# Kernel tuning notes

Measured on AMD Instinct MI355X. Metric: run time of the kernel, lower is better.

Reference implementation:

```python
import jax, jax.numpy as jnp
import numpy as np

NOISE_EPS = 0.01
TOP_K = 2


def setup_inputs() -> dict:
    key = jax.random.key(0)
    k1, k2, k3, k4 = jax.random.split(key, 4)
    B, S, D, E = 4, 4096, 2048, 64
    x = jax.random.normal(k1, (B, S, D), dtype=jnp.float32)
    raw_noise = jax.random.normal(k2, (B, S, E), dtype=jnp.float32)
    # gating_mlp: single Linear(D -> E), init std=0.02, zero bias
    W_gate = 0.02 * jax.random.normal(k3, (E, D), dtype=jnp.float32)
    b_gate = jnp.zeros((E,), dtype=jnp.float32)
    # noise_projection: Linear(D -> E, bias=False), init std=1/sqrt(D)
    W_noise = (1.0 / np.sqrt(D)) * jax.random.normal(k4, (E, D), dtype=jnp.float32)
    return {"x": x, "raw_noise": raw_noise, "W_gate": W_gate, "b_gate": b_gate, "W_noise": W_noise}


def reference(x, raw_noise, W_gate, b_gate, W_noise):
    # gate logits: [B,S,E]
    logits = jnp.einsum("bsd,ed->bse", x, W_gate) + b_gate
    # noisy top-k routing (training path)
    noise_stddev = jax.nn.softplus(jnp.einsum("bsd,ed->bse", x, W_noise)) + NOISE_EPS
    noisy = logits + raw_noise * noise_stddev
    top_v, top_i = jax.lax.top_k(noisy, TOP_K)            # [B,S,K]
    top_p = jax.nn.softmax(top_v.astype(jnp.float32), axis=-1).astype(noisy.dtype)
    B, S, E = noisy.shape
    T = B * S
    flat_logits = noisy.reshape(T, E)
    flat_i = top_i.reshape(T, TOP_K)
    flat_p = top_p.reshape(T, TOP_K)
    sparse = jnp.zeros((T, E), dtype=noisy.dtype).at[jnp.arange(T)[:, None], flat_i].set(flat_p)
    # aux load-balancing loss
    indicator = (sparse > 0.0).astype(jnp.float32)
    fraction_routed = indicator.sum(axis=0) / T           # f_e
    router_probs = jax.nn.softmax(flat_logits.astype(jnp.float32), axis=-1)
    avg_prob = router_probs.mean(axis=0)                  # p_e
    aux_loss = jnp.sum(fraction_routed * avg_prob) * E
    return sparse.reshape(B, S, E), aux_loss.astype(noisy.dtype)
```

## Files before the change

kernel.cpp:

```cpp
#include <hip/hip_runtime.h>
#include <math.h>

#define TOK 16384
#define DD  2048
#define EE  64
#define MT  32
#define BKC 32
#define NKC 64
#define LDA 40

typedef _Float16 half4v __attribute__((ext_vector_type(4)));
typedef _Float16 half8  __attribute__((ext_vector_type(8)));
typedef float    floatx4 __attribute__((ext_vector_type(4)));

__global__ void build_wf(const float* __restrict__ Wg, const float* __restrict__ Wn,
                         _Float16* __restrict__ wf) {
  int tid  = blockIdx.x * 256 + threadIdx.x;
  int lane = tid & 63;
  int kc   = (tid >> 6) & 63;
  int ct   = tid >> 12;
  int col  = (ct & 3) * 16 + (lane & 15);
  int k    = kc * 32 + (lane >> 4) * 8;
  const float* W = (ct < 4) ? Wg : Wn;
  const float* src = W + (size_t)col * DD + k;
  float4 a = *reinterpret_cast<const float4*>(src);
  float4 b = *reinterpret_cast<const float4*>(src + 4);
  float v[8] = {a.x, a.y, a.z, a.w, b.x, b.y, b.z, b.w};
  half8 hi, lo;
#pragma unroll
  for (int j = 0; j < 8; ++j) {
    _Float16 h = (_Float16)v[j];
    hi[j] = h;
    lo[j] = (_Float16)(v[j] - (float)h);
  }
  size_t base = (((size_t)(ct * 64 + kc) * 2 + 0) * 64 + lane) * 8;
  *reinterpret_cast<half8*>(wf + base)       = hi;
  *reinterpret_cast<half8*>(wf + base + 512) = lo;
}

__global__ __launch_bounds__(256, 2)
void gating_kernel(const float* __restrict__ x, const float* __restrict__ rn,
                   const _Float16* __restrict__ wf, const float* __restrict__ bg,
                   float* __restrict__ out,
                   float* __restrict__ cnt_g, float* __restrict__ psum_g) {
  __shared__ char smem[17536];
  _Float16* xs  = (_Float16*)smem;
  float*    Vb  = (float*)smem;
  float*    Eb  = (float*)(smem + 8448);
  float*    isum= (float*)(smem + 16896);
  int*      ti  = (int*)(smem + 17024);
  float*    tp  = (float*)(smem + 17280);

  const int t  = threadIdx.x;
  const int w  = t >> 6;
  const int l  = t & 63;
  const int q  = l >> 4;
  const int cl = l & 15;
  const int c  = w * 16 + cl;
  const int t0 = blockIdx.x * MT;

  const int stok = t >> 3;
  const int skof = (t & 7) * 4;
  const float* xrow = x + (size_t)(t0 + stok) * DD + skof;

  const float bgv = bg[c];
  float rnv[2][4];
#pragma unroll
  for (int mt = 0; mt < 2; ++mt)
#pragma unroll
    for (int r = 0; r < 4; ++r)
      rnv[mt][r] = rn[(size_t)(t0 + mt * 16 + q * 4 + r) * EE + c];

  floatx4 acc[2][2];
#pragma unroll
  for (int mt = 0; mt < 2; ++mt)
#pragma unroll
    for (int nt = 0; nt < 2; ++nt) acc[mt][nt] = (floatx4)0.f;

  const half8* wfp = (const half8*)wf;
  half8 Bc[2][2], Bn[2][2];

  {
    float4 a = *reinterpret_cast<const float4*>(xrow);
    float v[4] = {a.x, a.y, a.z, a.w};
    half4v hi, lo;
#pragma unroll
    for (int j = 0; j < 4; ++j) {
      _Float16 h = (_Float16)v[j];
      hi[j] = h;
      lo[j] = (_Float16)(v[j] - (float)h);
    }
    *reinterpret_cast<half4v*>(&xs[(0 * 2 + 0) * MT * LDA + stok * LDA + skof]) = hi;
    *reinterpret_cast<half4v*>(&xs[(0 * 2 + 1) * MT * LDA + stok * LDA + skof]) = lo;
#pragma unroll
    for (int nt = 0; nt < 2; ++nt) {
      const int ct = w + nt * 4;
#pragma unroll
      for (int s = 0; s < 2; ++s)
        Bc[nt][s] = wfp[((size_t)(ct * 64 + 0) * 2 + s) * 64 + l];
    }
  }

  for (int kc = 0; kc < NKC; ++kc) {
    const int cur = kc & 1;
    const bool more = (kc < NKC - 1);
    float4 pa;
    if (more) {
      pa = *reinterpret_cast<const float4*>(xrow + (kc + 1) * BKC);
#pragma unroll
      for (int nt = 0; nt < 2; ++nt) {
        const int ct = w + nt * 4;
#pragma unroll
        for (int s = 0; s < 2; ++s)
          Bn[nt][s] = wfp[((size_t)(ct * 64 + kc + 1) * 2 + s) * 64 + l];
      }
    }
    __syncthreads();

    half8 Ah[2], Al[2];
#pragma unroll
    for (int mt = 0; mt < 2; ++mt) {
      Ah[mt] = *reinterpret_cast<const half8*>(
          &xs[(cur * 2 + 0) * MT * LDA + (mt * 16 + cl) * LDA + q * 8]);
      Al[mt] = *reinterpret_cast<const half8*>(
          &xs[(cur * 2 + 1) * MT * LDA + (mt * 16 + cl) * LDA + q * 8]);
    }
#pragma unroll
    for (int mt = 0; mt < 2; ++mt)
#pragma unroll
      for (int nt = 0; nt < 2; ++nt)
        acc[mt][nt] = __builtin_amdgcn_mfma_f32_16x16x32_f16(Ah[mt], Bc[nt][0], acc[mt][nt], 0, 0, 0);
#pragma unroll
    for (int mt = 0; mt < 2; ++mt)
#pragma unroll
      for (int nt = 0; nt < 2; ++nt)
        acc[mt][nt] = __builtin_amdgcn_mfma_f32_16x16x32_f16(Ah[mt], Bc[nt][1], acc[mt][nt], 0, 0, 0);
#pragma unroll
    for (int mt = 0; mt < 2; ++mt)
#pragma unroll
      for (int nt = 0; nt < 2; ++nt)
        acc[mt][nt] = __builtin_amdgcn_mfma_f32_16x16x32_f16(Al[mt], Bc[nt][0], acc[mt][nt], 0, 0, 0);

    if (more) {
      float v[4] = {pa.x, pa.y, pa.z, pa.w};
      half4v hi, lo;
#pragma unroll
      for (int j = 0; j < 4; ++j) {
        _Float16 h = (_Float16)v[j];
        hi[j] = h;
        lo[j] = (_Float16)(v[j] - (float)h);
      }
      *reinterpret_cast<half4v*>(&xs[((cur ^ 1) * 2 + 0) * MT * LDA + stok * LDA + skof]) = hi;
      *reinterpret_cast<half4v*>(&xs[((cur ^ 1) * 2 + 1) * MT * LDA + stok * LDA + skof]) = lo;
#pragma unroll
      for (int nt = 0; nt < 2; ++nt)
#pragma unroll
        for (int s = 0; s < 2; ++s) Bc[nt][s] = Bn[nt][s];
    }
  }

  __syncthreads();

#pragma unroll
  for (int mt = 0; mt < 2; ++mt)
#pragma unroll
    for (int r = 0; r < 4; ++r) {
      const int tk = mt * 16 + q * 4 + r;
      float g  = acc[mt][0][r] + bgv;
      float h  = acc[mt][1][r];
      float sp = (h > 20.f) ? h : log1pf(expf(h));
      float v  = g + rnv[mt][r] * (sp + 0.01f);
      Vb[tk * 66 + c] = v;
      Eb[tk * 66 + c] = expf(v);
    }
  __syncthreads();

  if (t < MT) {
    float v1 = -1e30f, v2 = -1e30f;
    int   i1 = 0, i2 = 0;
    float s = 0.f;
    for (int e = 0; e < EE; ++e) {
      float v = Vb[t * 66 + e];
      s += Eb[t * 66 + e];
      if (v > v1)      { v2 = v1; i2 = i1; v1 = v; i1 = e; }
      else if (v > v2) { v2 = v;  i2 = e; }
    }
    isum[t] = 1.f / s;
    ti[t * 2 + 0] = i1; ti[t * 2 + 1] = i2;
    float e2 = expf(v2 - v1);
    float dn = 1.f + e2;
    tp[t * 2 + 0] = 1.f / dn;
    tp[t * 2 + 1] = e2 / dn;
  }
  __syncthreads();

  {
    const int m  = t >> 3;
    const int c0 = (t & 7) * 8;
    const int i1 = ti[m * 2 + 0], i2 = ti[m * 2 + 1];
    const float p1 = tp[m * 2 + 0], p2 = tp[m * 2 + 1];
    float o[8];
#pragma unroll
    for (int j = 0; j < 8; ++j) {
      const int col = c0 + j;
      o[j] = (col == i1) ? p1 : ((col == i2) ? p2 : 0.f);
    }
    float* dst = out + (size_t)(t0 + m) * EE + c0;
    *reinterpret_cast<float4*>(dst)     = make_float4(o[0], o[1], o[2], o[3]);
    *reinterpret_cast<float4*>(dst + 4) = make_float4(o[4], o[5], o[6], o[7]);
  }

  if (t < EE) {
    float s = 0.f;
    int   cn = 0;
#pragma unroll
    for (int m = 0; m < MT; ++m) {
      s  += Eb[m * 66 + t] * isum[m];
      cn += (ti[m * 2 + 0] == t) + (ti[m * 2 + 1] == t);
    }
    atomicAdd(&psum_g[t], s);
    atomicAdd(&cnt_g[t], (float)cn);
  }
}

__global__ void aux_kernel(const float* __restrict__ cnt_g,
                           const float* __restrict__ psum_g,
                           float* __restrict__ out) {
  int e = threadIdx.x;
  float v = cnt_g[e] * psum_g[e];
#pragma unroll
  for (int o = 32; o > 0; o >>= 1) v += __shfl_down(v, o);
  if (e == 0)
    out[(size_t)TOK * EE] = v * ((float)EE / ((float)TOK * (float)TOK));
}

extern "C" void kernel_launch(void* const* d_in, const int* in_sizes, int n_in,
                              void* d_out, int out_size, void* d_ws, size_t ws_size,
                              hipStream_t stream) {
  const float* x  = (const float*)d_in[0];
  const float* rn = (const float*)d_in[1];
  const float* Wg = (const float*)d_in[2];
  const float* bg = (const float*)d_in[3];
  const float* Wn = (const float*)d_in[4];
  float* out    = (float*)d_out;
  float* cnt_g  = (float*)d_ws;
  float* psum_g = cnt_g + EE;
  _Float16* wf  = (_Float16*)((float*)d_ws + 128);

  hipMemsetAsync(d_ws, 0, 2 * EE * sizeof(float), stream);
  build_wf<<<128, 256, 0, stream>>>(Wg, Wn, wf);
  gating_kernel<<<TOK / MT, 256, 0, stream>>>(x, rn, wf, bg, out, cnt_g, psum_g);
  aux_kernel<<<1, 64, 0, stream>>>(cnt_g, psum_g, out);
}
```

Baseline: 240.6 us.

## Split K across two warp groups per block and reduce partials in LDS

Doubles the block size to 512 threads and has each half process one half of the 2048-wide reduction dimension, so the per-block serial K loop is halved. Partial MFMA accumulators from the second group are written to shared memory and added by the first group before the softplus/top-k epilogue. The B-fragment double buffer is indexed by parity instead of copied, and the K loop is unrolled by 4. This adds more LDS, an extra reduction barrier, and higher register pressure per CU.

```diff
diff --git a/kernel.cpp b/kernel.cpp
--- a/kernel.cpp
+++ b/kernel.cpp
@@ -5,8 +5,8 @@
 #define DD  2048
 #define EE  64
 #define MT  32
-#define BKC 32
-#define NKC 64
+#define BK  32
+#define NKC 32
 #define LDA 40
 
 typedef _Float16 half4v __attribute__((ext_vector_type(4)));
@@ -38,47 +38,53 @@
   *reinterpret_cast<half8*>(wf + base + 512) = lo;
 }
 
-__global__ __launch_bounds__(256, 2)
+__global__ __launch_bounds__(512, 4)
 void gating_kernel(const float* __restrict__ x, const float* __restrict__ rn,
                    const _Float16* __restrict__ wf, const float* __restrict__ bg,
                    float* __restrict__ out,
                    float* __restrict__ cnt_g, float* __restrict__ psum_g) {
-  __shared__ char smem[17536];
-  _Float16* xs  = (_Float16*)smem;
-  float*    Vb  = (float*)smem;
-  float*    Eb  = (float*)(smem + 8448);
-  float*    isum= (float*)(smem + 16896);
-  int*      ti  = (int*)(smem + 17024);
-  float*    tp  = (float*)(smem + 17280);
+  __shared__ char smem[33920];
+  _Float16* xs   = (_Float16*)smem;
+  float*    Pacc = (float*)smem;
+  float*    Vb   = (float*)(smem + 16384);
+  float*    Eb   = (float*)(smem + 24832);
+  float*    isum = (float*)(smem + 33280);
+  int*      ti   = (int*)(smem + 33408);
+  float*    tp   = (float*)(smem + 33664);
 
   const int t  = threadIdx.x;
-  const int w  = t >> 6;
+  const int g  = t >> 8;
+  const int tg = t & 255;
+  const int w4 = tg >> 6;
   const int l  = t & 63;
   const int q  = l >> 4;
   const int cl = l & 15;
-  const int c  = w * 16 + cl;
+  const int c  = w4 * 16 + cl;
   const int t0 = blockIdx.x * MT;
 
-  const int stok = t >> 3;
-  const int skof = (t & 7) * 4;
-  const float* xrow = x + (size_t)(t0 + stok) * DD + skof;
-
-  const float bgv = bg[c];
-  float rnv[2][4];
+  const int stok = tg >> 3;
+  const int skof = (tg & 7) * 4;
+  const float* xrow = x + (size_t)(t0 + stok) * DD + g * (NKC * BK) + skof;
+
+  float bgv = 0.f;
+  float rnv[2][4] = {{0.f,0.f,0.f,0.f},{0.f,0.f,0.f,0.f}};
+  if (g == 0) {
+    bgv = bg[c];
+#pragma unroll
+    for (int mt = 0; mt < 2; ++mt)
+#pragma unroll
+      for (int r = 0; r < 4; ++r)
+        rnv[mt][r] = rn[(size_t)(t0 + mt * 16 + q * 4 + r) * EE + c];
+  }
+
+  floatx4 acc[2][2];
 #pragma unroll
   for (int mt = 0; mt < 2; ++mt)
 #pragma unroll
-    for (int r = 0; r < 4; ++r)
-      rnv[mt][r] = rn[(size_t)(t0 + mt * 16 + q * 4 + r) * EE + c];
-
-  floatx4 acc[2][2];
-#pragma unroll
-  for (int mt = 0; mt < 2; ++mt)
-#pragma unroll
     for (int nt = 0; nt < 2; ++nt) acc[mt][nt] = (floatx4)0.f;
 
   const half8* wfp = (const half8*)wf;
-  half8 Bc[2][2], Bn[2][2];
+  half8 B[2][2][2];
 
   {
     float4 a = *reinterpret_cast<const float4*>(xrow);
@@ -90,29 +96,30 @@
       hi[j] = h;
       lo[j] = (_Float16)(v[j] - (float)h);
     }
-    *reinterpret_cast<half4v*>(&xs[(0 * 2 + 0) * MT * LDA + stok * LDA + skof]) = hi;
-    *reinterpret_cast<half4v*>(&xs[(0 * 2 + 1) * MT * LDA + stok * LDA + skof]) = lo;
+    *reinterpret_cast<half4v*>(&xs[((g * 2 + 0) * 2 + 0) * (MT * LDA) + stok * LDA + skof]) = hi;
+    *reinterpret_cast<half4v*>(&xs[((g * 2 + 0) * 2 + 1) * (MT * LDA) + stok * LDA + skof]) = lo;
 #pragma unroll
     for (int nt = 0; nt < 2; ++nt) {
-      const int ct = w + nt * 4;
+      const int ct = w4 + nt * 4;
 #pragma unroll
       for (int s = 0; s < 2; ++s)
-        Bc[nt][s] = wfp[((size_t)(ct * 64 + 0) * 2 + s) * 64 + l];
-    }
-  }
-
+        B[0][nt][s] = wfp[((size_t)(ct * 64 + g * NKC) * 2 + s) * 64 + l];
+    }
+  }
+
+#pragma unroll 4
   for (int kc = 0; kc < NKC; ++kc) {
     const int cur = kc & 1;
     const bool more = (kc < NKC - 1);
     float4 pa;
     if (more) {
-      pa = *reinterpret_cast<const float4*>(xrow + (kc + 1) * BKC);
+      pa = *reinterpret_cast<const float4*>(xrow + (kc + 1) * BK);
 #pragma unroll
       for (int nt = 0; nt < 2; ++nt) {
-        const int ct = w + nt * 4;
+        const int ct = w4 + nt * 4;
 #pragma unroll
         for (int s = 0; s < 2; ++s)
-          Bn[nt][s] = wfp[((size_t)(ct * 64 + kc + 1) * 2 + s) * 64 + l];
+          B[cur ^ 1][nt][s] = wfp[((size_t)(ct * 64 + g * NKC + kc + 1) * 2 + s) * 64 + l];
       }
     }
     __syncthreads();
@@ -121,25 +128,25 @@
 #pragma unroll
     for (int mt = 0; mt < 2; ++mt) {
       Ah[mt] = *reinterpret_cast<const half8*>(
-          &xs[(cur * 2 + 0) * MT * LDA + (mt * 16 + cl) * LDA + q * 8]);
+          &xs[((g * 2 + cur) * 2 + 0) * (MT * LDA) + (mt * 16 + cl) * LDA + q * 8]);
       Al[mt] = *reinterpret_cast<const half8*>(
-          &xs[(cur * 2 + 1) * MT * LDA + (mt * 16 + cl) * LDA + q * 8]);
-    }
-#pragma unroll
-    for (int mt = 0; mt < 2; ++mt)
-#pragma unroll
-      for (int nt = 0; nt < 2; ++nt)
-        acc[mt][nt] = __builtin_amdgcn_mfma_f32_16x16x32_f16(Ah[mt], Bc[nt][0], acc[mt][nt], 0, 0, 0);
-#pragma unroll
-    for (int mt = 0; mt < 2; ++mt)
-#pragma unroll
-      for (int nt = 0; nt < 2; ++nt)
-        acc[mt][nt] = __builtin_amdgcn_mfma_f32_16x16x32_f16(Ah[mt], Bc[nt][1], acc[mt][nt], 0, 0, 0);
-#pragma unroll
-    for (int mt = 0; mt < 2; ++mt)
-#pragma unroll
-      for (int nt = 0; nt < 2; ++nt)
-        acc[mt][nt] = __builtin_amdgcn_mfma_f32_16x16x32_f16(Al[mt], Bc[nt][0], acc[mt][nt], 0, 0, 0);
+          &xs[((g * 2 + cur) * 2 + 1) * (MT * LDA) + (mt * 16 + cl) * LDA + q * 8]);
+    }
+#pragma unroll
+    for (int mt = 0; mt < 2; ++mt)
+#pragma unroll
+      for (int nt = 0; nt < 2; ++nt)
+        acc[mt][nt] = __builtin_amdgcn_mfma_f32_16x16x32_f16(Ah[mt], B[cur][nt][0], acc[mt][nt], 0, 0, 0);
+#pragma unroll
+    for (int mt = 0; mt < 2; ++mt)
+#pragma unroll
+      for (int nt = 0; nt < 2; ++nt)
+        acc[mt][nt] = __builtin_amdgcn_mfma_f32_16x16x32_f16(Ah[mt], B[cur][nt][1], acc[mt][nt], 0, 0, 0);
+#pragma unroll
+    for (int mt = 0; mt < 2; ++mt)
+#pragma unroll
+      for (int nt = 0; nt < 2; ++nt)
+        acc[mt][nt] = __builtin_amdgcn_mfma_f32_16x16x32_f16(Al[mt], B[cur][nt][0], acc[mt][nt], 0, 0, 0);
 
     if (more) {
       float v[4] = {pa.x, pa.y, pa.z, pa.w};
@@ -150,29 +157,46 @@
         hi[j] = h;
         lo[j] = (_Float16)(v[j] - (float)h);
       }
-      *reinterpret_cast<half4v*>(&xs[((cur ^ 1) * 2 + 0) * MT * LDA + stok * LDA + skof]) = hi;
-      *reinterpret_cast<half4v*>(&xs[((cur ^ 1) * 2 + 1) * MT * LDA + stok * LDA + skof]) = lo;
-#pragma unroll
-      for (int nt = 0; nt < 2; ++nt)
-#pragma unroll
-        for (int s = 0; s < 2; ++s) Bc[nt][s] = Bn[nt][s];
-    }
-  }
-
-  __syncthreads();
-
-#pragma unroll
-  for (int mt = 0; mt < 2; ++mt)
-#pragma unroll
-    for (int r = 0; r < 4; ++r) {
-      const int tk = mt * 16 + q * 4 + r;
-      float g  = acc[mt][0][r] + bgv;
-      float h  = acc[mt][1][r];
-      float sp = (h > 20.f) ? h : log1pf(expf(h));
-      float v  = g + rnv[mt][r] * (sp + 0.01f);
-      Vb[tk * 66 + c] = v;
-      Eb[tk * 66 + c] = expf(v);
-    }
+      *reinterpret_cast<half4v*>(&xs[((g * 2 + (cur ^ 1)) * 2 + 0) * (MT * LDA) + stok * LDA + skof]) = hi;
+      *reinterpret_cast<half4v*>(&xs[((g * 2 + (cur ^ 1)) * 2 + 1) * (MT * LDA) + stok * LDA + skof]) = lo;
+    }
+  }
+
+  __syncthreads();
+
+  if (g == 1) {
+#pragma unroll
+    for (int mt = 0; mt < 2; ++mt)
+#pragma unroll
+      for (int nt = 0; nt < 2; ++nt)
+#pragma unroll
+        for (int r = 0; r < 4; ++r)
+          Pacc[((((w4 * 2 + mt) * 2 + nt) * 4) + r) * 64 + l] = acc[mt][nt][r];
+  }
+  __syncthreads();
+
+  if (g == 0) {
+#pragma unroll
+    for (int mt = 0; mt < 2; ++mt)
+#pragma unroll
+      for (int nt = 0; nt < 2; ++nt)
+#pragma unroll
+        for (int r = 0; r < 4; ++r)
+          acc[mt][nt][r] += Pacc[((((w4 * 2 + mt) * 2 + nt) * 4) + r) * 64 + l];
+
+#pragma unroll
+    for (int mt = 0; mt < 2; ++mt)
+#pragma unroll
+      for (int r = 0; r < 4; ++r) {
+        const int tk = mt * 16 + q * 4 + r;
+        float gt = acc[mt][0][r] + bgv;
+        float h  = acc[mt][1][r];
+        float sp = (h > 20.f) ? h : log1pf(expf(h));
+        float v  = gt + rnv[mt][r] * (sp + 0.01f);
+        Vb[tk * 66 + c] = v;
+        Eb[tk * 66 + c] = expf(v);
+      }
+  }
   __syncthreads();
 
   if (t < MT) {
@@ -195,19 +219,18 @@
   __syncthreads();
 
   {
-    const int m  = t >> 3;
-    const int c0 = (t & 7) * 8;
+    const int m  = t >> 4;
+    const int c0 = (t & 15) * 4;
     const int i1 = ti[m * 2 + 0], i2 = ti[m * 2 + 1];
     const float p1 = tp[m * 2 + 0], p2 = tp[m * 2 + 1];
-    float o[8];
-#pragma unroll
-    for (int j = 0; j < 8; ++j) {
+    float o[4];
+#pragma unroll
+    for (int j = 0; j < 4; ++j) {
       const int col = c0 + j;
       o[j] = (col == i1) ? p1 : ((col == i2) ? p2 : 0.f);
     }
-    float* dst = out + (size_t)(t0 + m) * EE + c0;
-    *reinterpret_cast<float4*>(dst)     = make_float4(o[0], o[1], o[2], o[3]);
-    *reinterpret_cast<float4*>(dst + 4) = make_float4(o[4], o[5], o[6], o[7]);
+    *reinterpret_cast<float4*>(out + (size_t)(t0 + m) * EE + c0) =
+        make_float4(o[0], o[1], o[2], o[3]);
   }
 
   if (t < EE) {
@@ -249,6 +272,6 @@
 
   hipMemsetAsync(d_ws, 0, 2 * EE * sizeof(float), stream);
   build_wf<<<128, 256, 0, stream>>>(Wg, Wn, wf);
-  gating_kernel<<<TOK / MT, 256, 0, stream>>>(x, rn, wf, bg, out, cnt_g, psum_g);
+  gating_kernel<<<TOK / MT, 512, 0, stream>>>(x, rn, wf, bg, out, cnt_g, psum_g);
   aux_kernel<<<1, 64, 0, stream>>>(cnt_g, psum_g, out);
 }
```

Measured after the change: 235.7 us. -2.0%, faster.

## Split K across wave pairs and load x directly into registers without LDS

Applied to the files above, without the earlier changes.

The GEMM loop now splits the K dimension across two pairs of waves. Each wave covers 32 output columns for half of K and loads its x fragments straight from global memory into registers, doing the fp16 hi/lo split there. This removes the LDS staging of x and the per-iteration __syncthreads. The two K-halves are reduced through shared memory before the epilogue. In exchange, each x element is loaded by two waves, register pressure rises, and shared memory per block doubles, which may affect occupancy at launch_bounds(256,2).

```diff
diff --git a/kernel.cpp b/kernel.cpp
--- a/kernel.cpp
+++ b/kernel.cpp
@@ -5,11 +5,9 @@
 #define DD  2048
 #define EE  64
 #define MT  32
-#define BKC 32
-#define NKC 64
-#define LDA 40
-
-typedef _Float16 half4v __attribute__((ext_vector_type(4)));
+#define BK  32
+#define NKC 32
+
 typedef _Float16 half8  __attribute__((ext_vector_type(8)));
 typedef float    floatx4 __attribute__((ext_vector_type(4)));
 
@@ -43,136 +41,132 @@
                    const _Float16* __restrict__ wf, const float* __restrict__ bg,
                    float* __restrict__ out,
                    float* __restrict__ cnt_g, float* __restrict__ psum_g) {
-  __shared__ char smem[17536];
-  _Float16* xs  = (_Float16*)smem;
-  float*    Vb  = (float*)smem;
-  float*    Eb  = (float*)(smem + 8448);
-  float*    isum= (float*)(smem + 16896);
-  int*      ti  = (int*)(smem + 17024);
-  float*    tp  = (float*)(smem + 17280);
+  __shared__ char smem[34432];
+  float* Pacc = (float*)smem;
+  float* Vb   = (float*)(smem + 16896);
+  float* Eb   = (float*)(smem + 25344);
+  float* isum = (float*)(smem + 33792);
+  int*   ti   = (int*)(smem + 33920);
+  float* tp   = (float*)(smem + 34176);
 
   const int t  = threadIdx.x;
   const int w  = t >> 6;
+  const int ch = w & 1;
+  const int kh = w >> 1;
   const int l  = t & 63;
   const int q  = l >> 4;
   const int cl = l & 15;
-  const int c  = w * 16 + cl;
   const int t0 = blockIdx.x * MT;
 
-  const int stok = t >> 3;
-  const int skof = (t & 7) * 4;
-  const float* xrow = x + (size_t)(t0 + stok) * DD + skof;
-
-  const float bgv = bg[c];
-  float rnv[2][4];
+  const float* xr0 = x + (size_t)(t0 + cl) * DD + kh * (NKC * BK) + q * 8;
+  const float* xr1 = xr0 + (size_t)16 * DD;
+  const half8* wfp = (const half8*)wf;
+  const int cts[4] = {2 * ch, 2 * ch + 1, 4 + 2 * ch, 5 + 2 * ch};
+
+  floatx4 acc[2][4];
 #pragma unroll
   for (int mt = 0; mt < 2; ++mt)
 #pragma unroll
-    for (int r = 0; r < 4; ++r)
-      rnv[mt][r] = rn[(size_t)(t0 + mt * 16 + q * 4 + r) * EE + c];
-
-  floatx4 acc[2][2];
-#pragma unroll
-  for (int mt = 0; mt < 2; ++mt)
-#pragma unroll
-    for (int nt = 0; nt < 2; ++nt) acc[mt][nt] = (floatx4)0.f;
-
-  const half8* wfp = (const half8*)wf;
-  half8 Bc[2][2], Bn[2][2];
-
-  {
-    float4 a = *reinterpret_cast<const float4*>(xrow);
-    float v[4] = {a.x, a.y, a.z, a.w};
-    half4v hi, lo;
-#pragma unroll
-    for (int j = 0; j < 4; ++j) {
-      _Float16 h = (_Float16)v[j];
-      hi[j] = h;
-      lo[j] = (_Float16)(v[j] - (float)h);
-    }
-    *reinterpret_cast<half4v*>(&xs[(0 * 2 + 0) * MT * LDA + stok * LDA + skof]) = hi;
-    *reinterpret_cast<half4v*>(&xs[(0 * 2 + 1) * MT * LDA + stok * LDA + skof]) = lo;
-#pragma unroll
-    for (int nt = 0; nt < 2; ++nt) {
-      const int ct = w + nt * 4;
-#pragma unroll
-      for (int s = 0; s < 2; ++s)
-        Bc[nt][s] = wfp[((size_t)(ct * 64 + 0) * 2 + s) * 64 + l];
-    }
-  }
-
+    for (int j = 0; j < 4; ++j) acc[mt][j] = (floatx4)0.f;
+
+  float4 xr[2][2][2];
+  half8  Bf[2][4][2];
+
+#define LOAD_CHUNK(kc, p)                                                        \
+  {                                                                              \
+    const int off = (kc) * BK;                                                   \
+    xr[p][0][0] = *reinterpret_cast<const float4*>(xr0 + off);                   \
+    xr[p][0][1] = *reinterpret_cast<const float4*>(xr0 + off + 4);               \
+    xr[p][1][0] = *reinterpret_cast<const float4*>(xr1 + off);                   \
+    xr[p][1][1] = *reinterpret_cast<const float4*>(xr1 + off + 4);               \
+    const int kcg = kh * NKC + (kc);                                             \
+    _Pragma("unroll")                                                            \
+    for (int j = 0; j < 4; ++j) {                                                \
+      _Pragma("unroll")                                                          \
+      for (int s = 0; s < 2; ++s)                                                \
+        Bf[p][j][s] = wfp[((size_t)(cts[j] * 64 + kcg) * 2 + s) * 64 + l];       \
+    }                                                                            \
+  }
+
+  LOAD_CHUNK(0, 0)
+
+#pragma unroll 2
   for (int kc = 0; kc < NKC; ++kc) {
     const int cur = kc & 1;
-    const bool more = (kc < NKC - 1);
-    float4 pa;
-    if (more) {
-      pa = *reinterpret_cast<const float4*>(xrow + (kc + 1) * BKC);
-#pragma unroll
-      for (int nt = 0; nt < 2; ++nt) {
-        const int ct = w + nt * 4;
-#pragma unroll
-        for (int s = 0; s < 2; ++s)
-          Bn[nt][s] = wfp[((size_t)(ct * 64 + kc + 1) * 2 + s) * 64 + l];
+    if (kc + 1 < NKC) LOAD_CHUNK(kc + 1, cur ^ 1)
+
+    half8 Ah[2], Al[2];
+#pragma unroll
+    for (int mt = 0; mt < 2; ++mt) {
+      float v[8] = {xr[cur][mt][0].x, xr[cur][mt][0].y, xr[cur][mt][0].z, xr[cur][mt][0].w,
+                    xr[cur][mt][1].x, xr[cur][mt][1].y, xr[cur][mt][1].z, xr[cur][mt][1].w};
+#pragma unroll
+      for (int j = 0; j < 8; ++j) {
+        _Float16 h = (_Float16)v[j];
+        Ah[mt][j] = h;
+        Al[mt][j] = (_Float16)(v[j] - (float)h);
       }
     }
-    __syncthreads();
-
-    half8 Ah[2], Al[2];
-#pragma unroll
-    for (int mt = 0; mt < 2; ++mt) {
-      Ah[mt] = *reinterpret_cast<const half8*>(
-          &xs[(cur * 2 + 0) * MT * LDA + (mt * 16 + cl) * LDA + q * 8]);
-      Al[mt] = *reinterpret_cast<const half8*>(
-          &xs[(cur * 2 + 1) * MT * LDA + (mt * 16 + cl) * LDA + q * 8]);
-    }
-#pragma unroll
-    for (int mt = 0; mt < 2; ++mt)
-#pragma unroll
-      for (int nt = 0; nt < 2; ++nt)
-        acc[mt][nt] = __builtin_amdgcn_mfma_f32_16x16x32_f16(Ah[mt], Bc[nt][0], acc[mt][nt], 0, 0, 0);
-#pragma unroll
-    for (int mt = 0; mt < 2; ++mt)
-#pragma unroll
-      for (int nt = 0; nt < 2; ++nt)
-        acc[mt][nt] = __builtin_amdgcn_mfma_f32_16x16x32_f16(Ah[mt], Bc[nt][1], acc[mt][nt], 0, 0, 0);
-#pragma unroll
-    for (int mt = 0; mt < 2; ++mt)
-#pragma unroll
-      for (int nt = 0; nt < 2; ++nt)
-        acc[mt][nt] = __builtin_amdgcn_mfma_f32_16x16x32_f16(Al[mt], Bc[nt][0], acc[mt][nt], 0, 0, 0);
-
-    if (more) {
-      float v[4] = {pa.x, pa.y, pa.z, pa.w};
-      half4v hi, lo;
+#pragma unroll
+    for (int mt = 0; mt < 2; ++mt)
+#pragma unroll
+      for (int j = 0; j < 4; ++j)
+        acc[mt][j] = __builtin_amdgcn_mfma_f32_16x16x32_f16(Ah[mt], Bf[cur][j][0], acc[mt][j], 0, 0, 0);
+#pragma unroll
+    for (int mt = 0; mt < 2; ++mt)
+#pragma unroll
+      for (int j = 0; j < 4; ++j)
+        acc[mt][j] = __builtin_amdgcn_mfma_f32_16x16x32_f16(Ah[mt], Bf[cur][j][1], acc[mt][j], 0, 0, 0);
+#pragma unroll
+    for (int mt = 0; mt < 2; ++mt)
+#pragma unroll
+      for (int j = 0; j < 4; ++j)
+        acc[mt][j] = __builtin_amdgcn_mfma_f32_16x16x32_f16(Al[mt], Bf[cur][j][0], acc[mt][j], 0, 0, 0);
+  }
+#undef LOAD_CHUNK
+
+  if (kh == 1) {
+#pragma unroll
+    for (int mt = 0; mt < 2; ++mt)
 #pragma unroll
       for (int j = 0; j < 4; ++j) {
-        _Float16 h = (_Float16)v[j];
-        hi[j] = h;
-        lo[j] = (_Float16)(v[j] - (float)h);
+        const int cf = ((j >> 1) ? 64 : 0) + ch * 32 + (j & 1) * 16 + cl;
+#pragma unroll
+        for (int r = 0; r < 4; ++r)
+          Pacc[(mt * 16 + q * 4 + r) * 132 + cf] = acc[mt][j][r];
       }
-      *reinterpret_cast<half4v*>(&xs[((cur ^ 1) * 2 + 0) * MT * LDA + stok * LDA + skof]) = hi;
-      *reinterpret_cast<half4v*>(&xs[((cur ^ 1) * 2 + 1) * MT * LDA + stok * LDA + skof]) = lo;
-#pragma unroll
-      for (int nt = 0; nt < 2; ++nt)
-#pragma unroll
-        for (int s = 0; s < 2; ++s) Bc[nt][s] = Bn[nt][s];
-    }
-  }
-
+  }
   __syncthreads();
 
-#pragma unroll
-  for (int mt = 0; mt < 2; ++mt)
-#pragma unroll
-    for (int r = 0; r < 4; ++r) {
-      const int tk = mt * 16 + q * 4 + r;
-      float g  = acc[mt][0][r] + bgv;
-      float h  = acc[mt][1][r];
-      float sp = (h > 20.f) ? h : log1pf(expf(h));
-      float v  = g + rnv[mt][r] * (sp + 0.01f);
-      Vb[tk * 66 + c] = v;
-      Eb[tk * 66 + c] = expf(v);
-    }
+  if (kh == 0) {
+    float bgv[2], rnv[2][4][2];
+#pragma unroll
+    for (int j = 0; j < 2; ++j) bgv[j] = bg[ch * 32 + j * 16 + cl];
+#pragma unroll
+    for (int mt = 0; mt < 2; ++mt)
+#pragma unroll
+      for (int r = 0; r < 4; ++r)
+#pragma unroll
+        for (int j = 0; j < 2; ++j)
+          rnv[mt][r][j] = rn[(size_t)(t0 + mt * 16 + q * 4 + r) * EE + ch * 32 + j * 16 + cl];
+
+#pragma unroll
+    for (int mt = 0; mt < 2; ++mt)
+#pragma unroll
+      for (int r = 0; r < 4; ++r) {
+        const int tk = mt * 16 + q * 4 + r;
+#pragma unroll
+        for (int j = 0; j < 2; ++j) {
+          const int cg = ch * 32 + j * 16 + cl;
+          float g  = acc[mt][j][r]     + Pacc[tk * 132 + cg]      + bgv[j];
+          float h  = acc[mt][j + 2][r] + Pacc[tk * 132 + 64 + cg];
+          float sp = (h > 20.f) ? h : log1pf(expf(h));
+          float v  = g + rnv[mt][r][j] * (sp + 0.01f);
+          Vb[tk * 66 + cg] = v;
+          Eb[tk * 66 + cg] = expf(v);
+        }
+      }
+  }
   __syncthreads();
 
   if (t < MT) {
```

After: 250.2 us. 4.0% more time.
